# Performance work log

Hardware: AMD Instinct MI355X
Metric: run time of the kernel (lower is better)

The kernel has to match this reference:

```python
import jax, jax.numpy as jnp
import numpy as np

N_NODES = 100000
N_EDGES = 1600000
NUM_GRAPHS = 128
IN_F = 32
K = 3  # TAGConv default number of hops


def setup_inputs() -> dict:
    key = jax.random.key(0)
    ks = jax.random.split(key, 12)
    x = jax.random.normal(ks[0], (N_NODES, IN_F), dtype=jnp.float32)
    edge_index = jax.random.randint(ks[1], (2, N_EDGES), 0, N_NODES, dtype=jnp.int32)
    batch = jnp.sort(jax.random.randint(ks[2], (N_NODES,), 0, NUM_GRAPHS, dtype=jnp.int32))
    edge_weight = jax.random.uniform(ks[3], (N_EDGES,), dtype=jnp.float32)
    # TAGConv params: K+1 weight matrices per layer (bias shared per layer)
    s1 = 1.0 / np.sqrt(IN_F)
    s2 = 1.0 / np.sqrt(8)
    s3 = 1.0 / np.sqrt(32)
    W1 = jax.random.uniform(ks[4], (K + 1, IN_F, 8), jnp.float32, -s1, s1)
    b1 = jax.random.uniform(ks[5], (8,), jnp.float32, -s1, s1)
    W2 = jax.random.uniform(ks[6], (K + 1, 8, 16), jnp.float32, -s2, s2)
    b2 = jax.random.uniform(ks[7], (16,), jnp.float32, -s2, s2)
    Wfc = jax.random.uniform(ks[8], (32, 2), jnp.float32, -s3, s3)
    bfc = jax.random.uniform(ks[9], (2,), jnp.float32, -s3, s3)
    return {"x": x, "edge_index": edge_index, "batch": batch, "edge_weight": edge_weight,
            "W1": W1, "b1": b1, "W2": W2, "b2": b2, "Wfc": Wfc, "bfc": bfc}


def reference(x, edge_index, batch, edge_weight, W1, b1, W2, b2, Wfc, bfc):
    src, dst = edge_index[0], edge_index[1]
    n = x.shape[0]
    # gcn_norm without self-loops (TAGConv default): D^-1/2 A D^-1/2
    deg = jax.ops.segment_sum(edge_weight, dst, num_segments=n)
    dinv = jnp.where(deg > 0, jax.lax.rsqrt(jnp.maximum(deg, 1e-30)), 0.0)
    norm = dinv[src] * edge_weight * dinv[dst]

    def tag_conv(h, W, b):
        out = h @ W[0]
        for k in range(1, W.shape[0]):
            # sparse propagate: gather at src, scale, scatter-add at dst
            h = jax.ops.segment_sum(h[src] * norm[:, None], dst, num_segments=n)
            out = out + h @ W[k]
        return out + b

    h = jax.nn.relu(tag_conv(x, W1, b1))
    h = jax.nn.relu(tag_conv(h, W2, b2))
    # global max pool + global mean pool over graphs in the batch
    mx = jax.ops.segment_max(h, batch, num_segments=NUM_GRAPHS)
    cnt = jax.ops.segment_sum(jnp.ones((n,), h.dtype), batch, num_segments=NUM_GRAPHS)
    mean = jax.ops.segment_sum(h, batch, num_segments=NUM_GRAPHS) / jnp.maximum(cnt, 1.0)[:, None]
    return jnp.concatenate([mx, mean], axis=1) @ Wfc + bfc
```

## Files before the change

### kernel.cpp

```cpp
#include <hip/hip_runtime.h>

constexpr int NN = 100000;
constexpr int NE = 1600000;
constexpr int NG = 128;

constexpr int SCAN_T = 256;
constexpr int SCAN_B = (NN + SCAN_T - 1) / SCAN_T;

struct __align__(8) Ent { int s; float nw; };


__global__ void k_rank(const int4* __restrict__ dst4, int* __restrict__ cnt,
                       ushort4* __restrict__ rank4, int ne4) {
    int i = blockIdx.x * blockDim.x + threadIdx.x;
    if (i >= ne4) return;
    int4 d = dst4[i];
    ushort4 r;
    r.x = (ushort)atomicAdd(&cnt[d.x], 1);
    r.y = (ushort)atomicAdd(&cnt[d.y], 1);
    r.z = (ushort)atomicAdd(&cnt[d.z], 1);
    r.w = (ushort)atomicAdd(&cnt[d.w], 1);
    rank4[i] = r;
}


__global__ void k_scan1(const int* __restrict__ cnt, int* __restrict__ bsum, int nn) {
    __shared__ int s[SCAN_T];
    int i = blockIdx.x * SCAN_T + threadIdx.x;
    s[threadIdx.x] = (i < nn) ? ((cnt[i] + 1) & ~1) : 0;
    __syncthreads();
    for (int off = SCAN_T / 2; off > 0; off >>= 1) {
        if (threadIdx.x < off) s[threadIdx.x] += s[threadIdx.x + off];
        __syncthreads();
    }
    if (threadIdx.x == 0) bsum[blockIdx.x] = s[0];
}

__global__ void k_scan2(int* __restrict__ bsum, int nb) {
    __shared__ int s[512];
    int t = threadIdx.x;
    s[t] = (t < nb) ? bsum[t] : 0;
    __syncthreads();
    for (int off = 1; off < 512; off <<= 1) {
        int v = (t >= off) ? s[t - off] : 0;
        __syncthreads();
        s[t] += v;
        __syncthreads();
    }
    if (t < nb) bsum[t] = (t > 0) ? s[t - 1] : 0;
}

__global__ void k_scan3(const int* __restrict__ cnt, const int* __restrict__ bsum,
                        int* __restrict__ row_ptr, int nn) {
    __shared__ int s[SCAN_T];
    int t = threadIdx.x;
    int i = blockIdx.x * SCAN_T + t;
    int v = (i < nn) ? ((cnt[i] + 1) & ~1) : 0;
    s[t] = v;
    __syncthreads();
    for (int off = 1; off < SCAN_T; off <<= 1) {
        int u = (t >= off) ? s[t - off] : 0;
        __syncthreads();
        s[t] += u;
        __syncthreads();
    }
    int incl = s[t];
    int base = bsum[blockIdx.x];
    if (i < nn) {
        row_ptr[i] = base + incl - v;
        if (i == nn - 1) row_ptr[nn] = base + incl;
    }
}

__global__ void k_scatter2(const int4* __restrict__ src4, const int4* __restrict__ dst4,
                           const float4* __restrict__ w4, const int* __restrict__ row_ptr,
                           const ushort4* __restrict__ rank4, Ent* __restrict__ csr, int ne4) {
    int i = blockIdx.x * blockDim.x + threadIdx.x;
    if (i >= ne4) return;
    int4 s = src4[i]; int4 d = dst4[i]; float4 w = w4[i]; ushort4 r = rank4[i];
    Ent e0; e0.s = s.x; e0.nw = w.x; csr[row_ptr[d.x] + r.x] = e0;
    Ent e1; e1.s = s.y; e1.nw = w.y; csr[row_ptr[d.y] + r.y] = e1;
    Ent e2; e2.s = s.z; e2.nw = w.z; csr[row_ptr[d.z] + r.z] = e2;
    Ent e3; e3.s = s.w; e3.nw = w.w; csr[row_ptr[d.w] + r.w] = e3;
}

__global__ void k_pad(const int* __restrict__ cnt, const int* __restrict__ row_ptr,
                      Ent* __restrict__ csr, int nn) {
    int n = blockIdx.x * blockDim.x + threadIdx.x;
    if (n < nn && (cnt[n] & 1)) {
        Ent z; z.s = 0; z.nw = 0.f;
        csr[row_ptr[n] + cnt[n]] = z;
    }
}

__global__ void k_degi(const int* __restrict__ row_ptr, const float4* __restrict__ csr4,
                       float* __restrict__ dinv, int nn) {
    int tid = blockIdx.x * blockDim.x + threadIdx.x;
    int n = tid >> 3, lane = tid & 7;
    if (n >= nn) return;
    int beg = row_ptr[n] >> 1, end = row_ptr[n + 1] >> 1;
    float s = 0.f;
    for (int p = beg + lane; p < end; p += 8) {
        float4 a = csr4[p];
        s += a.y + a.w;
    }
    s += __shfl_xor(s, 1, 64);
    s += __shfl_xor(s, 2, 64);
    s += __shfl_xor(s, 4, 64);
    if (lane == 0) dinv[n] = s > 0.f ? rsqrtf(fmaxf(s, 1e-30f)) : 0.f;
}

template <int FIN, int FOUT>
__global__ void k_mm4(const float* __restrict__ h, const float* __restrict__ W,
                      const float* __restrict__ dinv, float* __restrict__ t, int nn) {
    __shared__ float sW[4 * FIN * FOUT];
    for (int i = threadIdx.x; i < 4 * FIN * FOUT; i += blockDim.x) sW[i] = W[i];
    __syncthreads();
    int n = blockIdx.x * blockDim.x + threadIdx.x;
    if (n >= nn) return;
    float hr[FIN];
    const float4* hp = reinterpret_cast<const float4*>(h + (size_t)n * FIN);
#pragma unroll
    for (int f = 0; f < FIN / 4; ++f) {
        float4 v = hp[f];
        hr[4 * f + 0] = v.x; hr[4 * f + 1] = v.y;
        hr[4 * f + 2] = v.z; hr[4 * f + 3] = v.w;
    }
    float dv = dinv[n];
#pragma unroll
    for (int k = 0; k < 4; ++k) {
        float acc[FOUT];
#pragma unroll
        for (int j = 0; j < FOUT; ++j) acc[j] = 0.f;
#pragma unroll
        for (int i = 0; i < FIN; ++i) {
            float hv = hr[i];
            const float* wrow = &sW[(k * FIN + i) * FOUT];
#pragma unroll
            for (int j = 0; j < FOUT; ++j) acc[j] = fmaf(hv, wrow[j], acc[j]);
        }
        if (k == 3) {
#pragma unroll
            for (int j = 0; j < FOUT; ++j) acc[j] *= dv;
        }
        float4* op = reinterpret_cast<float4*>(t + ((size_t)k * nn + n) * FOUT);
#pragma unroll
        for (int j4 = 0; j4 < FOUT / 4; ++j4)
            op[j4] = make_float4(acc[4 * j4], acc[4 * j4 + 1], acc[4 * j4 + 2], acc[4 * j4 + 3]);
    }
}

template <int F, bool FINAL>
__global__ void k_pull(const int* __restrict__ row_ptr, const float4* __restrict__ csr4,
                       const float* __restrict__ dinv,
                       const float* __restrict__ hin, const float* __restrict__ add,
                       const float* __restrict__ b, float* __restrict__ hout, int nn) {
    int g = blockIdx.x * (blockDim.x / F) + threadIdx.x / F;
    int lane = threadIdx.x & (F - 1);
    if (g >= nn) return;
    int p = row_ptr[g] >> 1, end = row_ptr[g + 1] >> 1;
    float acc0 = 0.f, acc1 = 0.f, acc2 = 0.f, acc3 = 0.f;
    for (; p + 2 <= end; p += 2) {
        float4 a = csr4[p], c = csr4[p + 1];
        acc0 = fmaf(hin[(size_t)__float_as_int(a.x) * F + lane], a.y, acc0);
        acc1 = fmaf(hin[(size_t)__float_as_int(a.z) * F + lane], a.w, acc1);
        acc2 = fmaf(hin[(size_t)__float_as_int(c.x) * F + lane], c.y, acc2);
        acc3 = fmaf(hin[(size_t)__float_as_int(c.z) * F + lane], c.w, acc3);
    }
    if (p < end) {
        float4 a = csr4[p];
        acc0 = fmaf(hin[(size_t)__float_as_int(a.x) * F + lane], a.y, acc0);
        acc1 = fmaf(hin[(size_t)__float_as_int(a.z) * F + lane], a.w, acc1);
    }
    float acc = (acc0 + acc1) + (acc2 + acc3);
    float dv = dinv[g];
    float r;
    if (FINAL) r = fmaxf(dv * acc + add[(size_t)g * F + lane] + b[lane], 0.f);
    else       r = dv * (dv * acc + add[(size_t)g * F + lane]);
    hout[(size_t)g * F + lane] = r;
}


__global__ void k_bounds(const int* __restrict__ batch, int* __restrict__ start, int nn) {
    int i = blockIdx.x * blockDim.x + threadIdx.x;
    if (i >= nn) return;
    int b = batch[i];
    int prev = (i == 0) ? -1 : batch[i - 1];
    for (int g = prev + 1; g <= b; ++g) start[g] = i;
    if (i == nn - 1) {
        for (int g = b + 1; g <= NG; ++g) start[g] = nn;
    }
}

__global__ void k_pool2(const float* __restrict__ h, const int* __restrict__ start,
                        const float* __restrict__ Wfc, const float* __restrict__ bfc,
                        float* __restrict__ out) {
    int g = blockIdx.x;
    int beg = start[g], end = start[g + 1];
    int tid = threadIdx.x;
    int feat = tid & 15, grp = tid >> 4;
    float mx = 0.f, sm = 0.f;
    for (int n = beg + grp; n < end; n += 16) {
        float v = h[(size_t)n * 16 + feat];
        mx = fmaxf(mx, v);
        sm += v;
    }
    mx = fmaxf(mx, __shfl_xor(mx, 16, 64));
    sm += __shfl_xor(sm, 16, 64);
    mx = fmaxf(mx, __shfl_xor(mx, 32, 64));
    sm += __shfl_xor(sm, 32, 64);
    __shared__ float smx[4][16], ssm[4][16];
    int wave = tid >> 6;
    int lane = tid & 63;
    if (lane < 16) { smx[wave][feat] = mx; ssm[wave][feat] = sm; }
    __syncthreads();
    if (tid < 16) {
        float m = fmaxf(fmaxf(smx[0][tid], smx[1][tid]), fmaxf(smx[2][tid], smx[3][tid]));
        float s = ssm[0][tid] + ssm[1][tid] + ssm[2][tid] + ssm[3][tid];
        smx[0][tid] = m;
        ssm[0][tid] = (end > beg) ? s / (float)(end - beg) : 0.f;
    }
    __syncthreads();
    if (tid < 2) {
        float acc = bfc[tid];
#pragma unroll
        for (int i = 0; i < 16; ++i) acc += smx[0][i] * Wfc[i * 2 + tid];
#pragma unroll
        for (int i = 0; i < 16; ++i) acc += ssm[0][i] * Wfc[(16 + i) * 2 + tid];
        out[g * 2 + tid] = acc;
    }
}


extern "C" void kernel_launch(void* const* d_in, const int* in_sizes, int n_in,
                              void* d_out, int out_size, void* d_ws, size_t ws_size,
                              hipStream_t stream) {
    const float* x    = (const float*)d_in[0];
    const int*   eidx = (const int*)d_in[1];
    const int*   srcp = eidx;
    const int*   dstp = eidx + NE;
    const int*   batch= (const int*)d_in[2];
    const float* ew   = (const float*)d_in[3];
    const float* W1   = (const float*)d_in[4];
    const float* b1   = (const float*)d_in[5];
    const float* W2   = (const float*)d_in[6];
    const float* b2   = (const float*)d_in[7];
    const float* Wfc  = (const float*)d_in[8];
    const float* bfc  = (const float*)d_in[9];
    float* out = (float*)d_out;

    constexpr size_t NN8  = (size_t)NN * 8;
    constexpr size_t NN16 = (size_t)NN * 16;

    float*  dinv    = (float*)d_ws;
    int*    cnt     = (int*)(dinv + NN);
    int*    row_ptr = cnt + NN;
    ushort* rank    = (ushort*)(row_ptr + NN + 4);
    Ent*    csr     = (Ent*)((int*)(void*)rank + NE / 2);
    float*  uni     = (float*)(csr + NE + NN);
    float*  h1      = uni + 5 * NN16;
    int*    gstart  = (int*)(h1 + NN8);
    int*    bsum    = gstart + NG + 4;

    float* T  = uni;
    float* P  = uni + 2 * NN16;
    float* P2 = P + NN8;
    float* U    = uni;
    float* q    = uni + 4 * NN16;
    float* q2   = U + 3 * NN16;
    float* out2 = U + 2 * NN16;

    const float4* csr4 = (const float4*)csr;

    const int BLK = 256;
    const int NE4 = NE / 4;
    const int gE4 = (NE4 + BLK - 1) / BLK;
    const int gN  = (NN + BLK - 1) / BLK;
    const int gP8  = (NN + (BLK / 8) - 1) / (BLK / 8);
    const int gP16 = (NN + (BLK / 16) - 1) / (BLK / 16);
    const int gN8  = (NN * 8 + BLK - 1) / BLK;

    hipMemsetAsync(cnt, 0, (size_t)NN * sizeof(int), stream);
    k_rank<<<gE4, BLK, 0, stream>>>((const int4*)dstp, cnt, (ushort4*)rank, NE4);
    k_scan1<<<SCAN_B, SCAN_T, 0, stream>>>(cnt, bsum, NN);
    k_scan2<<<1, 512, 0, stream>>>(bsum, SCAN_B);
    k_scan3<<<SCAN_B, SCAN_T, 0, stream>>>(cnt, bsum, row_ptr, NN);
    k_scatter2<<<gE4, BLK, 0, stream>>>((const int4*)srcp, (const int4*)dstp,
                                        (const float4*)ew, row_ptr, (const ushort4*)rank,
                                        csr, NE4);
    k_pad<<<gN, BLK, 0, stream>>>(cnt, row_ptr, csr, NN);
    k_degi<<<gN8, BLK, 0, stream>>>(row_ptr, csr4, dinv, NN);
    k_bounds<<<gN, BLK, 0, stream>>>(batch, gstart, NN);

    k_mm4<32, 8><<<gN, BLK, 0, stream>>>(x, W1, dinv, T, NN);
    k_pull<8, false><<<gP8, BLK, 0, stream>>>(row_ptr, csr4, dinv, T + 3 * NN8, T + 2 * NN8, nullptr, P, NN);
    k_pull<8, false><<<gP8, BLK, 0, stream>>>(row_ptr, csr4, dinv, P, T + 1 * NN8, nullptr, P2, NN);
    k_pull<8, true ><<<gP8, BLK, 0, stream>>>(row_ptr, csr4, dinv, P2, T, b1, h1, NN);

    k_mm4<8, 16><<<gN, BLK, 0, stream>>>(h1, W2, dinv, U, NN);
    k_pull<16, false><<<gP16, BLK, 0, stream>>>(row_ptr, csr4, dinv, U + 3 * NN16, U + 2 * NN16, nullptr, q, NN);
    k_pull<16, false><<<gP16, BLK, 0, stream>>>(row_ptr, csr4, dinv, q, U + 1 * NN16, nullptr, q2, NN);
    k_pull<16, true ><<<gP16, BLK, 0, stream>>>(row_ptr, csr4, dinv, q2, U, b2, out2, NN);

    k_pool2<<<NG, 256, 0, stream>>>(out2, gstart, Wfc, bfc, out);
}
```

Before: 309.8 us.

## Fuse front kernels, fold padding into scan, vectorize pull gathers with float4

Merges edge ranking, the first-layer feature transform and graph-bound detection into one launch with block-range dispatch. The CSR padding write moves into the scan kernel, and the dinv scaling of the first layer's last hop moves into the degree kernel. The pull kernels now have each thread gather float4 chunks instead of single floats, so each node uses fewer threads. This cuts launch count and per-element gather instructions, at the cost of fewer concurrent threads per node and larger per-thread loads.

```diff
diff --git a/kernel.cpp b/kernel.cpp
--- a/kernel.cpp
+++ b/kernel.cpp
@@ -4,23 +4,72 @@
 constexpr int NE = 1600000;
 constexpr int NG = 128;
 
+constexpr int BLK = 256;
+constexpr int NE4 = NE / 4;
+constexpr int G_RANK = (NE4 + BLK - 1) / BLK;
+constexpr int G_N    = (NN + BLK - 1) / BLK;
+
 constexpr int SCAN_T = 256;
 constexpr int SCAN_B = (NN + SCAN_T - 1) / SCAN_T;
 
 struct __align__(8) Ent { int s; float nw; };
 
 
-__global__ void k_rank(const int4* __restrict__ dst4, int* __restrict__ cnt,
-                       ushort4* __restrict__ rank4, int ne4) {
-    int i = blockIdx.x * blockDim.x + threadIdx.x;
-    if (i >= ne4) return;
-    int4 d = dst4[i];
-    ushort4 r;
-    r.x = (ushort)atomicAdd(&cnt[d.x], 1);
-    r.y = (ushort)atomicAdd(&cnt[d.y], 1);
-    r.z = (ushort)atomicAdd(&cnt[d.z], 1);
-    r.w = (ushort)atomicAdd(&cnt[d.w], 1);
-    rank4[i] = r;
+__global__ void k_front(const int4* __restrict__ dst4, int* __restrict__ cnt,
+                        ushort4* __restrict__ rank4,
+                        const float* __restrict__ x, const float* __restrict__ W1,
+                        float* __restrict__ T,
+                        const int* __restrict__ batch, int* __restrict__ gstart) {
+    __shared__ float sW[4 * 32 * 8];
+    int b = blockIdx.x;
+    if (b < G_RANK) {
+        int i = b * BLK + threadIdx.x;
+        if (i >= NE4) return;
+        int4 d = dst4[i];
+        ushort4 r;
+        r.x = (ushort)atomicAdd(&cnt[d.x], 1);
+        r.y = (ushort)atomicAdd(&cnt[d.y], 1);
+        r.z = (ushort)atomicAdd(&cnt[d.z], 1);
+        r.w = (ushort)atomicAdd(&cnt[d.w], 1);
+        rank4[i] = r;
+    } else if (b < G_RANK + G_N) {
+        for (int i = threadIdx.x; i < 4 * 32 * 8; i += BLK) sW[i] = W1[i];
+        __syncthreads();
+        int n = (b - G_RANK) * BLK + threadIdx.x;
+        if (n >= NN) return;
+        float hr[32];
+        const float4* hp = reinterpret_cast<const float4*>(x + (size_t)n * 32);
+#pragma unroll
+        for (int f = 0; f < 8; ++f) {
+            float4 v = hp[f];
+            hr[4 * f] = v.x; hr[4 * f + 1] = v.y; hr[4 * f + 2] = v.z; hr[4 * f + 3] = v.w;
+        }
+#pragma unroll
+        for (int k = 0; k < 4; ++k) {
+            float acc[8];
+#pragma unroll
+            for (int j = 0; j < 8; ++j) acc[j] = 0.f;
+#pragma unroll
+            for (int i = 0; i < 32; ++i) {
+                float hv = hr[i];
+                const float* wrow = &sW[(k * 32 + i) * 8];
+#pragma unroll
+                for (int j = 0; j < 8; ++j) acc[j] = fmaf(hv, wrow[j], acc[j]);
+            }
+            float4* op = reinterpret_cast<float4*>(T + ((size_t)k * NN + n) * 8);
+            op[0] = make_float4(acc[0], acc[1], acc[2], acc[3]);
+            op[1] = make_float4(acc[4], acc[5], acc[6], acc[7]);
+        }
+    } else {
+        int i = (b - G_RANK - G_N) * BLK + threadIdx.x;
+        if (i >= NN) return;
+        int bb = batch[i];
+        int prev = (i == 0) ? -1 : batch[i - 1];
+        for (int g = prev + 1; g <= bb; ++g) gstart[g] = i;
+        if (i == NN - 1) {
+            for (int g = bb + 1; g <= NG; ++g) gstart[g] = NN;
+        }
+    }
 }
 
 
@@ -51,11 +100,12 @@
 }
 
 __global__ void k_scan3(const int* __restrict__ cnt, const int* __restrict__ bsum,
-                        int* __restrict__ row_ptr, int nn) {
+                        int* __restrict__ row_ptr, Ent* __restrict__ csr, int nn) {
     __shared__ int s[SCAN_T];
     int t = threadIdx.x;
     int i = blockIdx.x * SCAN_T + t;
-    int v = (i < nn) ? ((cnt[i] + 1) & ~1) : 0;
+    int c0 = (i < nn) ? cnt[i] : 0;
+    int v = (c0 + 1) & ~1;
     s[t] = v;
     __syncthreads();
     for (int off = 1; off < SCAN_T; off <<= 1) {
@@ -67,8 +117,13 @@
     int incl = s[t];
     int base = bsum[blockIdx.x];
     if (i < nn) {
-        row_ptr[i] = base + incl - v;
+        int rp = base + incl - v;
+        row_ptr[i] = rp;
         if (i == nn - 1) row_ptr[nn] = base + incl;
+        if (c0 & 1) {
+            Ent z; z.s = 0; z.nw = 0.f;
+            csr[rp + c0] = z;
+        }
     }
 }
 
@@ -84,17 +139,8 @@
     Ent e3; e3.s = s.w; e3.nw = w.w; csr[row_ptr[d.w] + r.w] = e3;
 }
 
-__global__ void k_pad(const int* __restrict__ cnt, const int* __restrict__ row_ptr,
-                      Ent* __restrict__ csr, int nn) {
-    int n = blockIdx.x * blockDim.x + threadIdx.x;
-    if (n < nn && (cnt[n] & 1)) {
-        Ent z; z.s = 0; z.nw = 0.f;
-        csr[row_ptr[n] + cnt[n]] = z;
-    }
-}
-
 __global__ void k_degi(const int* __restrict__ row_ptr, const float4* __restrict__ csr4,
-                       float* __restrict__ dinv, int nn) {
+                       float* __restrict__ dinv, float4* __restrict__ T3, int nn) {
     int tid = blockIdx.x * blockDim.x + threadIdx.x;
     int n = tid >> 3, lane = tid & 7;
     if (n >= nn) return;
@@ -107,45 +153,48 @@
     s += __shfl_xor(s, 1, 64);
     s += __shfl_xor(s, 2, 64);
     s += __shfl_xor(s, 4, 64);
-    if (lane == 0) dinv[n] = s > 0.f ? rsqrtf(fmaxf(s, 1e-30f)) : 0.f;
-}
-
-template <int FIN, int FOUT>
-__global__ void k_mm4(const float* __restrict__ h, const float* __restrict__ W,
-                      const float* __restrict__ dinv, float* __restrict__ t, int nn) {
-    __shared__ float sW[4 * FIN * FOUT];
-    for (int i = threadIdx.x; i < 4 * FIN * FOUT; i += blockDim.x) sW[i] = W[i];
+    float dv = s > 0.f ? rsqrtf(fmaxf(s, 1e-30f)) : 0.f;
+    if (lane == 0) dinv[n] = dv;
+    if (lane < 2) {
+        float4 t = T3[(size_t)n * 2 + lane];
+        T3[(size_t)n * 2 + lane] = make_float4(t.x * dv, t.y * dv, t.z * dv, t.w * dv);
+    }
+}
+
+__global__ void k_mm4b(const float* __restrict__ h, const float* __restrict__ W,
+                       const float* __restrict__ dinv, float* __restrict__ t, int nn) {
+    __shared__ float sW[4 * 8 * 16];
+    for (int i = threadIdx.x; i < 4 * 8 * 16; i += blockDim.x) sW[i] = W[i];
     __syncthreads();
     int n = blockIdx.x * blockDim.x + threadIdx.x;
     if (n >= nn) return;
-    float hr[FIN];
-    const float4* hp = reinterpret_cast<const float4*>(h + (size_t)n * FIN);
-#pragma unroll
-    for (int f = 0; f < FIN / 4; ++f) {
+    float hr[8];
+    const float4* hp = reinterpret_cast<const float4*>(h + (size_t)n * 8);
+#pragma unroll
+    for (int f = 0; f < 2; ++f) {
         float4 v = hp[f];
-        hr[4 * f + 0] = v.x; hr[4 * f + 1] = v.y;
-        hr[4 * f + 2] = v.z; hr[4 * f + 3] = v.w;
+        hr[4 * f] = v.x; hr[4 * f + 1] = v.y; hr[4 * f + 2] = v.z; hr[4 * f + 3] = v.w;
     }
     float dv = dinv[n];
 #pragma unroll
     for (int k = 0; k < 4; ++k) {
-        float acc[FOUT];
-#pragma unroll
-        for (int j = 0; j < FOUT; ++j) acc[j] = 0.f;
-#pragma unroll
-        for (int i = 0; i < FIN; ++i) {
+        float acc[16];
+#pragma unroll
+        for (int j = 0; j < 16; ++j) acc[j] = 0.f;
+#pragma unroll
+        for (int i = 0; i < 8; ++i) {
             float hv = hr[i];
-            const float* wrow = &sW[(k * FIN + i) * FOUT];
-#pragma unroll
-            for (int j = 0; j < FOUT; ++j) acc[j] = fmaf(hv, wrow[j], acc[j]);
+            const float* wrow = &sW[(k * 8 + i) * 16];
+#pragma unroll
+            for (int j = 0; j < 16; ++j) acc[j] = fmaf(hv, wrow[j], acc[j]);
         }
         if (k == 3) {
 #pragma unroll
-            for (int j = 0; j < FOUT; ++j) acc[j] *= dv;
-        }
-        float4* op = reinterpret_cast<float4*>(t + ((size_t)k * nn + n) * FOUT);
-#pragma unroll
-        for (int j4 = 0; j4 < FOUT / 4; ++j4)
+            for (int j = 0; j < 16; ++j) acc[j] *= dv;
+        }
+        float4* op = reinterpret_cast<float4*>(t + ((size_t)k * nn + n) * 16);
+#pragma unroll
+        for (int j4 = 0; j4 < 4; ++j4)
             op[j4] = make_float4(acc[4 * j4], acc[4 * j4 + 1], acc[4 * j4 + 2], acc[4 * j4 + 3]);
     }
 }
@@ -153,44 +202,43 @@
 template <int F, bool FINAL>
 __global__ void k_pull(const int* __restrict__ row_ptr, const float4* __restrict__ csr4,
                        const float* __restrict__ dinv,
-                       const float* __restrict__ hin, const float* __restrict__ add,
-                       const float* __restrict__ b, float* __restrict__ hout, int nn) {
-    int g = blockIdx.x * (blockDim.x / F) + threadIdx.x / F;
-    int lane = threadIdx.x & (F - 1);
+                       const float4* __restrict__ hin4, const float4* __restrict__ add4,
+                       const float* __restrict__ b, float4* __restrict__ hout4, int nn) {
+    constexpr int P = F / 4;
+    int g = blockIdx.x * (blockDim.x / P) + threadIdx.x / P;
+    int c = threadIdx.x & (P - 1);
     if (g >= nn) return;
     int p = row_ptr[g] >> 1, end = row_ptr[g + 1] >> 1;
-    float acc0 = 0.f, acc1 = 0.f, acc2 = 0.f, acc3 = 0.f;
-    for (; p + 2 <= end; p += 2) {
-        float4 a = csr4[p], c = csr4[p + 1];
-        acc0 = fmaf(hin[(size_t)__float_as_int(a.x) * F + lane], a.y, acc0);
-        acc1 = fmaf(hin[(size_t)__float_as_int(a.z) * F + lane], a.w, acc1);
-        acc2 = fmaf(hin[(size_t)__float_as_int(c.x) * F + lane], c.y, acc2);
-        acc3 = fmaf(hin[(size_t)__float_as_int(c.z) * F + lane], c.w, acc3);
-    }
-    if (p < end) {
+    float4 A = make_float4(0.f, 0.f, 0.f, 0.f);
+    float4 B = make_float4(0.f, 0.f, 0.f, 0.f);
+    for (; p < end; ++p) {
         float4 a = csr4[p];
-        acc0 = fmaf(hin[(size_t)__float_as_int(a.x) * F + lane], a.y, acc0);
-        acc1 = fmaf(hin[(size_t)__float_as_int(a.z) * F + lane], a.w, acc1);
-    }
-    float acc = (acc0 + acc1) + (acc2 + acc3);
+        int s0 = __float_as_int(a.x), s1 = __float_as_int(a.z);
+        float4 h0 = hin4[(size_t)s0 * P + c];
+        float4 h1 = hin4[(size_t)s1 * P + c];
+        A.x = fmaf(h0.x, a.y, A.x); A.y = fmaf(h0.y, a.y, A.y);
+        A.z = fmaf(h0.z, a.y, A.z); A.w = fmaf(h0.w, a.y, A.w);
+        B.x = fmaf(h1.x, a.w, B.x); B.y = fmaf(h1.y, a.w, B.y);
+        B.z = fmaf(h1.z, a.w, B.z); B.w = fmaf(h1.w, a.w, B.w);
+    }
     float dv = dinv[g];
-    float r;
-    if (FINAL) r = fmaxf(dv * acc + add[(size_t)g * F + lane] + b[lane], 0.f);
-    else       r = dv * (dv * acc + add[(size_t)g * F + lane]);
-    hout[(size_t)g * F + lane] = r;
-}
-
-
-__global__ void k_bounds(const int* __restrict__ batch, int* __restrict__ start, int nn) {
-    int i = blockIdx.x * blockDim.x + threadIdx.x;
-    if (i >= nn) return;
-    int b = batch[i];
-    int prev = (i == 0) ? -1 : batch[i - 1];
-    for (int g = prev + 1; g <= b; ++g) start[g] = i;
-    if (i == nn - 1) {
-        for (int g = b + 1; g <= NG; ++g) start[g] = nn;
-    }
-}
+    float4 ad = add4[(size_t)g * P + c];
+    float4 r;
+    if (FINAL) {
+        float4 bb = reinterpret_cast<const float4*>(b)[c];
+        r.x = fmaxf(dv * (A.x + B.x) + ad.x + bb.x, 0.f);
+        r.y = fmaxf(dv * (A.y + B.y) + ad.y + bb.y, 0.f);
+        r.z = fmaxf(dv * (A.z + B.z) + ad.z + bb.z, 0.f);
+        r.w = fmaxf(dv * (A.w + B.w) + ad.w + bb.w, 0.f);
+    } else {
+        r.x = dv * (dv * (A.x + B.x) + ad.x);
+        r.y = dv * (dv * (A.y + B.y) + ad.y);
+        r.z = dv * (dv * (A.z + B.z) + ad.z);
+        r.w = dv * (dv * (A.w + B.w) + ad.w);
+    }
+    hout4[(size_t)g * P + c] = r;
+}
+
 
 __global__ void k_pool2(const float* __restrict__ h, const int* __restrict__ start,
                         const float* __restrict__ Wfc, const float* __restrict__ bfc,
@@ -272,35 +320,35 @@
 
     const float4* csr4 = (const float4*)csr;
 
-    const int BLK = 256;
-    const int NE4 = NE / 4;
-    const int gE4 = (NE4 + BLK - 1) / BLK;
-    const int gN  = (NN + BLK - 1) / BLK;
-    const int gP8  = (NN + (BLK / 8) - 1) / (BLK / 8);
-    const int gP16 = (NN + (BLK / 16) - 1) / (BLK / 16);
+    const int gP8  = (NN + (BLK / 2) - 1) / (BLK / 2);
+    const int gP16 = (NN + (BLK / 4) - 1) / (BLK / 4);
     const int gN8  = (NN * 8 + BLK - 1) / BLK;
 
     hipMemsetAsync(cnt, 0, (size_t)NN * sizeof(int), stream);
-    k_rank<<<gE4, BLK, 0, stream>>>((const int4*)dstp, cnt, (ushort4*)rank, NE4);
+    k_front<<<G_RANK + 2 * G_N, BLK, 0, stream>>>((const int4*)dstp, cnt, (ushort4*)rank,
+                                                  x, W1, T, batch, gstart);
     k_scan1<<<SCAN_B, SCAN_T, 0, stream>>>(cnt, bsum, NN);
     k_scan2<<<1, 512, 0, stream>>>(bsum, SCAN_B);
-    k_scan3<<<SCAN_B, SCAN_T, 0, stream>>>(cnt, bsum, row_ptr, NN);
-    k_scatter2<<<gE4, BLK, 0, stream>>>((const int4*)srcp, (const int4*)dstp,
-                                        (const float4*)ew, row_ptr, (const ushort4*)rank,
-                                        csr, NE4);
-    k_pad<<<gN, BLK, 0, stream>>>(cnt, row_ptr, csr, NN);
-    k_degi<<<gN8, BLK, 0, stream>>>(row_ptr, csr4, dinv, NN);
-    k_bounds<<<gN, BLK, 0, stream>>>(batch, gstart, NN);
-
-    k_mm4<32, 8><<<gN, BLK, 0, stream>>>(x, W1, dinv, T, NN);
-    k_pull<8, false><<<gP8, BLK, 0, stream>>>(row_ptr, csr4, dinv, T + 3 * NN8, T + 2 * NN8, nullptr, P, NN);
-    k_pull<8, false><<<gP8, BLK, 0, stream>>>(row_ptr, csr4, dinv, P, T + 1 * NN8, nullptr, P2, NN);
-    k_pull<8, true ><<<gP8, BLK, 0, stream>>>(row_ptr, csr4, dinv, P2, T, b1, h1, NN);
-
-    k_mm4<8, 16><<<gN, BLK, 0, stream>>>(h1, W2, dinv, U, NN);
-    k_pull<16, false><<<gP16, BLK, 0, stream>>>(row_ptr, csr4, dinv, U + 3 * NN16, U + 2 * NN16, nullptr, q, NN);
-    k_pull<16, false><<<gP16, BLK, 0, stream>>>(row_ptr, csr4, dinv, q, U + 1 * NN16, nullptr, q2, NN);
-    k_pull<16, true ><<<gP16, BLK, 0, stream>>>(row_ptr, csr4, dinv, q2, U, b2, out2, NN);
+    k_scan3<<<SCAN_B, SCAN_T, 0, stream>>>(cnt, bsum, row_ptr, csr, NN);
+    k_scatter2<<<G_RANK, BLK, 0, stream>>>((const int4*)srcp, (const int4*)dstp,
+                                           (const float4*)ew, row_ptr, (const ushort4*)rank,
+                                           csr, NE4);
+    k_degi<<<gN8, BLK, 0, stream>>>(row_ptr, csr4, dinv, (float4*)(T + 3 * NN8), NN);
+
+    k_pull<8, false><<<gP8, BLK, 0, stream>>>(row_ptr, csr4, dinv, (const float4*)(T + 3 * NN8),
+                                              (const float4*)(T + 2 * NN8), nullptr, (float4*)P, NN);
+    k_pull<8, false><<<gP8, BLK, 0, stream>>>(row_ptr, csr4, dinv, (const float4*)P,
+                                              (const float4*)(T + 1 * NN8), nullptr, (float4*)P2, NN);
+    k_pull<8, true ><<<gP8, BLK, 0, stream>>>(row_ptr, csr4, dinv, (const float4*)P2,
+                                              (const float4*)T, b1, (float4*)h1, NN);
+
+    k_mm4b<<<G_N, BLK, 0, stream>>>(h1, W2, dinv, U, NN);
+    k_pull<16, false><<<gP16, BLK, 0, stream>>>(row_ptr, csr4, dinv, (const float4*)(U + 3 * NN16),
+                                                (const float4*)(U + 2 * NN16), nullptr, (float4*)q, NN);
+    k_pull<16, false><<<gP16, BLK, 0, stream>>>(row_ptr, csr4, dinv, (const float4*)q,
+                                                (const float4*)(U + 1 * NN16), nullptr, (float4*)q2, NN);
+    k_pull<16, true ><<<gP16, BLK, 0, stream>>>(row_ptr, csr4, dinv, (const float4*)q2,
+                                                (const float4*)U, b2, (float4*)out2, NN);
 
     k_pool2<<<NG, 256, 0, stream>>>(out2, gstart, Wfc, bfc, out);
 }
```

New measurement: 342.8 us. 1.11x slower.
